# Performance work log

Hardware: AMD Instinct MI355X
Metric: run time of the kernel (lower is better)

The kernel has to match this reference:

```python
import jax, jax.numpy as jnp
import numpy as np

D_MODEL = 256
N_HEAD = 4
N_LAYERS = 2
D_FF = 4 * D_MODEL
VOCAB = 4096
DINO = 384
T_SEQ = 40
N_PATCH = 256
B = 32
LN_EPS = 1e-5


def setup_inputs() -> dict:
    key = jax.random.key(0)
    ks = jax.random.split(key, 24)
    f = jnp.float32
    d = {}
    d['patches'] = jax.random.normal(ks[0], (B, N_PATCH, DINO), dtype=f)
    d['tokens'] = jax.random.randint(ks[1], (B, T_SEQ), 0, VOCAB)
    s = 0.02
    d['embedding'] = jax.random.normal(ks[2], (VOCAB, D_MODEL), dtype=f) * s
    d['pos_emb'] = jax.random.normal(ks[3], (T_SEQ, D_MODEL), dtype=f) * s
    d['in_proj_w'] = jax.random.normal(ks[4], (N_LAYERS, 3 * D_MODEL, D_MODEL), dtype=f) * s
    d['in_proj_b'] = jnp.zeros((N_LAYERS, 3 * D_MODEL), dtype=f)
    d['out_proj_w'] = jax.random.normal(ks[5], (N_LAYERS, D_MODEL, D_MODEL), dtype=f) * s
    d['out_proj_b'] = jnp.zeros((N_LAYERS, D_MODEL), dtype=f)
    d['lin1_w'] = jax.random.normal(ks[6], (N_LAYERS, D_FF, D_MODEL), dtype=f) * s
    d['lin1_b'] = jnp.zeros((N_LAYERS, D_FF), dtype=f)
    d['lin2_w'] = jax.random.normal(ks[7], (N_LAYERS, D_MODEL, D_FF), dtype=f) * s
    d['lin2_b'] = jnp.zeros((N_LAYERS, D_MODEL), dtype=f)
    d['ln1_g'] = jnp.ones((N_LAYERS, D_MODEL), dtype=f)
    d['ln1_b'] = jnp.zeros((N_LAYERS, D_MODEL), dtype=f)
    d['ln2_g'] = jnp.ones((N_LAYERS, D_MODEL), dtype=f)
    d['ln2_b'] = jnp.zeros((N_LAYERS, D_MODEL), dtype=f)
    d['fus_w1'] = jax.random.normal(ks[8], (D_MODEL, DINO + D_MODEL), dtype=f) * s
    d['fus_b1'] = jnp.zeros((D_MODEL,), dtype=f)
    d['fus_w2'] = jax.random.normal(ks[9], (D_MODEL, D_MODEL), dtype=f) * s
    d['fus_b2'] = jnp.zeros((D_MODEL,), dtype=f)
    d['cls_w'] = jax.random.normal(ks[10], (VOCAB, D_MODEL), dtype=f) * s
    d['cls_b'] = jnp.zeros((VOCAB,), dtype=f)
    return d


def _layer_norm(x, g, b):
    m = jnp.mean(x, axis=-1, keepdims=True)
    v = jnp.mean((x - m) ** 2, axis=-1, keepdims=True)
    return (x - m) / jnp.sqrt(v + LN_EPS) * g + b


def _encode(x, mask, in_proj_w, in_proj_b, out_proj_w, out_proj_b,
            lin1_w, lin1_b, lin2_w, lin2_b, ln1_g, ln1_b, ln2_g, ln2_b):
    # x: [N, S, d], mask: [N, S] bool (True = valid key). Post-norm encoder, relu FFN.
    N, S, d = x.shape
    hd = d // N_HEAD
    for i in range(N_LAYERS):
        qkv = x @ in_proj_w[i].T + in_proj_b[i]
        q, k, v = jnp.split(qkv, 3, axis=-1)
        sh = lambda t: t.reshape(N, S, N_HEAD, hd).transpose(0, 2, 1, 3)
        q, k, v = sh(q), sh(k), sh(v)
        sc = jnp.einsum('nhqd,nhkd->nhqk', q, k) / np.sqrt(hd)
        sc = jnp.where(mask[:, None, None, :], sc, -1e9)
        a = jax.nn.softmax(sc, axis=-1)
        o = jnp.einsum('nhqk,nhkd->nhqd', a, v).transpose(0, 2, 1, 3).reshape(N, S, d)
        o = o @ out_proj_w[i].T + out_proj_b[i]
        x = _layer_norm(x + o, ln1_g[i], ln1_b[i])
        ff = jax.nn.relu(x @ lin1_w[i].T + lin1_b[i]) @ lin2_w[i].T + lin2_b[i]
        x = _layer_norm(x + ff, ln2_g[i], ln2_b[i])
    return x


def reference(patches, tokens, embedding, pos_emb, in_proj_w, in_proj_b,
              out_proj_w, out_proj_b, lin1_w, lin1_b, lin2_w, lin2_b,
              ln1_g, ln1_b, ln2_g, ln2_b, fus_w1, fus_b1, fus_w2, fus_b2,
              cls_w, cls_b):
    Bsz, T = tokens.shape
    d = embedding.shape[1]
    emb = embedding[tokens] + pos_emb[None, :T, :]      # [B, T, d]
    Tm1 = T - 1
    # All 39 prefix runs at once: prefix of length t+1 == full seq with keys > t masked.
    X = jnp.broadcast_to(emb[None], (Tm1, Bsz, T, d)).reshape(Tm1 * Bsz, T, d)
    valid = jnp.arange(T)[None, :] <= jnp.arange(Tm1)[:, None]  # [Tm1, T]
    mask = jnp.broadcast_to(valid[:, None, :], (Tm1, Bsz, T)).reshape(Tm1 * Bsz, T)
    enc = _encode(X, mask, in_proj_w, in_proj_b, out_proj_w, out_proj_b,
                  lin1_w, lin1_b, lin2_w, lin2_b, ln1_g, ln1_b, ln2_g, ln2_b)
    enc = enc.reshape(Tm1, Bsz, T, d)
    idx = jnp.arange(Tm1)
    ctx_rest = enc[idx, :, idx, :]                      # [Tm1, B, d] last valid position
    ctx = jnp.concatenate([jnp.zeros((1, Bsz, d), emb.dtype), ctx_rest], axis=0)  # [T, B, d]
    # Fusion MLP: split first linear into patch part (t-invariant) + context part.
    w1p, w1c = fus_w1[:, :DINO], fus_w1[:, DINO:]
    pp = jnp.einsum('bpd,kd->bpk', patches, w1p)        # [B, P, d]
    cp = jnp.einsum('tbd,kd->tbk', ctx, w1c) + fus_b1   # [T, B, d]
    h = jax.nn.gelu(pp[None] + cp[:, :, None, :], approximate=False)  # [T, B, P, d]
    feat = jnp.einsum('tbpk,mk->tbpm', h, fus_w2) + fus_b2            # [T, B, P, d]
    # Gather-only classification: prob of tokens[:, t] at step t.
    targets = tokens.T                                   # [T, B]
    cw = cls_w[targets]                                  # [T, B, d]
    cb = cls_b[targets]                                  # [T, B]
    logits = jnp.einsum('tbpm,tbm->tbp', feat, cw) + cb[:, :, None]
    probs = jax.nn.sigmoid(logits)                       # [T, B, P]
    return probs.transpose(1, 2, 0)                      # [B, P, T]
```

## Files before the change

kernel.cpp:

```cpp
#include <hip/hip_runtime.h>
#include <math.h>

#define DM    256
#define NH    4
#define HD    64
#define TS    40
#define TM1   39
#define BB    32
#define DFF   1024
#define DINO  384
#define NPATCH 256
#define VOCAB 4096

#define NTOK  24960
#define NQ2   1248

typedef _Float16 f16;
typedef __attribute__((ext_vector_type(8))) _Float16 half8;
typedef __attribute__((ext_vector_type(4))) _Float16 half4;
typedef __attribute__((ext_vector_type(4))) float f32x4;

#define OFF_EMBH   0u
#define OFF_EMB    163840u
#define OFF_QKVH   491520u
#define OFF_X1     983040u
#define OFF_X1H    7372800u
#define OFF_H1     10567680u
#define OFF_BIG    16957440u
#define   BT_AO1H  6389760u
#define   BT_X2    6553600u
#define   BT_X2H   6881280u
#define   BT_FF2H  7045120u
#define   BT_H1H   7700480u
#define OFF_CTX    29736960u
#define OFF_CPB    30064640u
#define OFF_U      30392320u
#define OFF_S      30720000u
#define OFF_WQKVH  30722048u
#define OFF_WQ1H   30820352u
#define OFF_KVWH   30853120u
#define OFF_WOH    30918656u
#define OFF_WOH1   30951424u
#define OFF_L1WH   30984192u
#define OFF_L1WH1  31115264u
#define OFF_L2WH   31246336u
#define OFF_L2WH1  31377408u
#define OFF_W1PH   31508480u
#define OFF_W1CH   31557632u
#define OFF_FW2TH  31590400u
#define OFF_CWGH   31623168u
#define OFF_MAP    31787008u
#define WS_FLOATS  31813216u

__global__ __launch_bounds__(256) void prep_kernel(
    const int* __restrict__ tokens, const float* __restrict__ etab,
    const float* __restrict__ pos,
    const float* __restrict__ ipw, const float* __restrict__ opw,
    const float* __restrict__ l1w, const float* __restrict__ l2w,
    const float* __restrict__ fw1, const float* __restrict__ fw2,
    const float* __restrict__ clsw, const float* __restrict__ clsb,
    const float* __restrict__ fb2,
    float* __restrict__ emb, f16* __restrict__ embh,
    f16* __restrict__ wqkvh, f16* __restrict__ wq1h, f16* __restrict__ kvwh,
    f16* __restrict__ woh, f16* __restrict__ woh1,
    f16* __restrict__ l1wh, f16* __restrict__ l1wh1,
    f16* __restrict__ l2wh, f16* __restrict__ l2wh1,
    f16* __restrict__ w1ph, f16* __restrict__ w1ch, f16* __restrict__ fw2th,
    f16* __restrict__ cwgh, float* __restrict__ sv, float* __restrict__ ctx,
    int* __restrict__ map1, int* __restrict__ map2)
{
    int i = blockIdx.x * 256 + threadIdx.x;
    if (i < 327680) {
        int r = i >> 8, j = i & 255;
        int p = r % TS;
        float v = etab[(size_t)tokens[r] * DM + j] + pos[p * DM + j];
        emb[i] = v; embh[i] = (f16)v;
        return;
    }
    i -= 327680;
    if (i < 196608) { wqkvh[i] = (f16)ipw[i]; return; }
    i -= 196608;
    if (i < 65536)  { wq1h[i] = (f16)ipw[196608 + i]; return; }
    i -= 65536;
    if (i < 131072) { kvwh[i] = (f16)ipw[262144 + i]; return; }
    i -= 131072;
    if (i < 65536)  { woh[i]  = (f16)opw[i]; return; }
    i -= 65536;
    if (i < 65536)  { woh1[i] = (f16)opw[65536 + i]; return; }
    i -= 65536;
    if (i < 262144) { l1wh[i]  = (f16)l1w[i]; return; }
    i -= 262144;
    if (i < 262144) { l1wh1[i] = (f16)l1w[262144 + i]; return; }
    i -= 262144;
    if (i < 262144) { l2wh[i]  = (f16)l2w[i]; return; }
    i -= 262144;
    if (i < 262144) { l2wh1[i] = (f16)l2w[262144 + i]; return; }
    i -= 262144;
    if (i < 98304) {
        int r = i / 384, c = i - r * 384;
        w1ph[i] = (f16)fw1[r * 640 + c];
        return;
    }
    i -= 98304;
    if (i < 65536) {
        int n = i >> 8, k = i & 255;
        w1ch[i] = (f16)fw1[n * 640 + 384 + k];
        return;
    }
    i -= 65536;
    if (i < 65536) {
        int j = i >> 8, k = i & 255;
        fw2th[i] = (f16)fw2[k * 256 + j];
        return;
    }
    i -= 65536;
    if (i < 327680) {
        int tb = i >> 8, j = i & 255;
        int t = tb >> 5, b = tb & 31;
        cwgh[i] = (f16)clsw[(size_t)tokens[b * TS + t] * DM + j];
        return;
    }
    i -= 327680;
    if (i < 81920) {
        int tb = i >> 6, l = i & 63;
        int t = tb >> 5, b = tb & 31;
        int tok = tokens[b * TS + t];
        float a = 0.f;
#pragma unroll
        for (int c = 0; c < 4; ++c)
            a += fb2[l + 64 * c] * clsw[(size_t)tok * DM + l + 64 * c];
#pragma unroll
        for (int o = 32; o; o >>= 1) a += __shfl_xor(a, o);
        if (l == 0) sv[tb] = a + clsb[tok];
        return;
    }
    i -= 81920;
    if (i < 8192) { ctx[i] = 0.f; return; }
    i -= 8192;
    if (i < NQ2) {
        int t = i >> 5, b = i & 31;
        map2[i] = ((t * (t + 1)) / 2 + t) * 32 + b;
    }
    if (i < NTOK) {
        int q = i >> 5, b = i & 31;
        int t = 0;
        while (((t + 1) * (t + 2)) / 2 <= q) ++t;
        int p = q - (t * (t + 1)) / 2;
        map1[i] = b * TS + p;
    }
}

__device__ __forceinline__ void stage16(const f16* g, f16* lbase_wave_uniform) {
    __builtin_amdgcn_global_load_lds(
        (const __attribute__((address_space(1))) void*)g,
        (__attribute__((address_space(3))) void*)lbase_wave_uniform, 16, 0, 0);
}

__device__ __forceinline__ half8 load_frag8(const float* p) {
    float4 a0 = *(const float4*)p;
    float4 a1 = *(const float4*)(p + 4);
    half8 h;
    h[0] = (f16)a0.x; h[1] = (f16)a0.y; h[2] = (f16)a0.z; h[3] = (f16)a0.w;
    h[4] = (f16)a1.x; h[5] = (f16)a1.y; h[6] = (f16)a1.z; h[7] = (f16)a1.w;
    return h;
}

template <int BM, typename TA, bool RELU, bool OUTF16>
__global__ __launch_bounds__(256) void gemm_x(
    const TA* __restrict__ A, int lda,
    const f16* __restrict__ B, int ldb,
    const float* __restrict__ bias,
    void* __restrict__ Cv, int ldc, int K)
{
    constexpr int AF  = BM / 8;
    constexpr int TF  = AF + 16;
    constexpr int MRE = BM / 32;
    constexpr int LPW = TF / 4;
    constexpr bool ASYNC = __is_same(TA, f16);
    constexpr int NBUF = ASYNC ? 2 : 1;
    __shared__ __align__(16) f16 lds[NBUF * TF * 512];
    int tid = threadIdx.x;
    int w = tid >> 6, l = tid & 63;
    int m0 = blockIdx.y * BM, n0 = blockIdx.x << 7;
    int lrow = l & 15;
    int lk8  = (l >> 4) << 3;
    int wm = w >> 1, wn = w & 1;

    f32x4 acc[MRE][4] = {};

    auto stage = [&](f16* dst, int k0) {
#pragma unroll
        for (int j = 0; j < TF / 4; ++j) {
            int f = (j << 2) | w;
            if (f < AF) {
                int mi = f >> 1, kc = f & 1;
                const TA* ga = A + (size_t)(m0 + (mi << 4) + lrow) * lda + k0 + (kc << 5) + lk8;
                if constexpr (ASYNC) {
                    stage16((const f16*)ga, dst + (f << 9));
                } else {
                    *(half8*)&dst[(f << 9) + (l << 3)] = load_frag8((const float*)ga);
                }
            } else {
                int fb = f - AF;
                int nj = fb >> 1, kc = fb & 1;
                const f16* gb = B + (size_t)(n0 + (nj << 4) + lrow) * ldb + k0 + (kc << 5) + lk8;
                stage16(gb, dst + (f << 9));
            }
        }
    };

    auto compute = [&](const f16* buf) {
#pragma unroll
        for (int kc = 0; kc < 2; ++kc) {
            half8 af[MRE], bfr[4];
#pragma unroll
            for (int i = 0; i < MRE; ++i)
                af[i] = *(const half8*)&buf[((((wm * MRE + i) << 1) | kc) << 9) + (l << 3)];
#pragma unroll
            for (int j2 = 0; j2 < 4; ++j2)
                bfr[j2] = *(const half8*)&buf[((AF + ((((wn << 2) | j2) << 1) | kc)) << 9) + (l << 3)];
#pragma unroll
            for (int i = 0; i < MRE; ++i)
#pragma unroll
                for (int j2 = 0; j2 < 4; ++j2)
                    acc[i][j2] = __builtin_amdgcn_mfma_f32_16x16x32_f16(
                        af[i], bfr[j2], acc[i][j2], 0, 0, 0);
        }
    };

    if constexpr (ASYNC) {
        int nk = K >> 6;
        stage(lds, 0);
        for (int t = 0; t < nk; ++t) {
            f16* cur = lds + (t & 1) * (TF * 512);
            if (t + 1 < nk) {
                stage(lds + ((t + 1) & 1) * (TF * 512), (t + 1) << 6);
                asm volatile("s_waitcnt vmcnt(%0)" :: "i"(LPW) : "memory");
            } else {
                asm volatile("s_waitcnt vmcnt(0)" ::: "memory");
            }
            __builtin_amdgcn_s_barrier();
            asm volatile("" ::: "memory");
            compute(cur);
            asm volatile("" ::: "memory");
            __builtin_amdgcn_s_barrier();
            asm volatile("" ::: "memory");
        }
    } else {
        for (int k0 = 0; k0 < K; k0 += 64) {
            stage(lds, k0);
            __syncthreads();
            compute(lds);
            __syncthreads();
        }
    }

    int colq = l & 15, rowq = (l >> 4) << 2;
#pragma unroll
    for (int i = 0; i < MRE; ++i) {
        int gmb = m0 + (wm * MRE + i) * 16 + rowq;
#pragma unroll
        for (int j2 = 0; j2 < 4; ++j2) {
            int gn = n0 + ((wn << 2) | j2) * 16 + colq;
            float bv = bias ? bias[gn] : 0.f;
#pragma unroll
            for (int r = 0; r < 4; ++r) {
                float v = acc[i][j2][r] + bv;
                if (RELU) v = fmaxf(v, 0.f);
                if (OUTF16)
                    ((f16*)Cv)[(size_t)(gmb + r) * ldc + gn] = (f16)v;
                else
                    ((float*)Cv)[(size_t)(gmb + r) * ldc + gn] = v;
            }
        }
    }
}

__global__ __launch_bounds__(256) void ln_kernel(
    float* __restrict__ X, const float* __restrict__ res,
    const int* __restrict__ map, const float* __restrict__ g,
    const float* __restrict__ beta, int nrows, f16* __restrict__ outh)
{
    int r = blockIdx.x * 4 + (threadIdx.x >> 6);
    if (r >= nrows) return;
    int l = threadIdx.x & 63;
    float* xp = X + (size_t)r * DM + l * 4;
    float4 v = *(float4*)xp;
    if (res) {
        int rr = map ? map[r] : r;
        float4 rv = *(const float4*)(res + (size_t)rr * DM + l * 4);
        v.x += rv.x; v.y += rv.y; v.z += rv.z; v.w += rv.w;
    }
    float s = v.x + v.y + v.z + v.w;
#pragma unroll
    for (int o = 32; o; o >>= 1) s += __shfl_xor(s, o);
    float mean = s * (1.f / 256.f);
    float dx = v.x - mean, dy = v.y - mean, dz = v.z - mean, dw = v.w - mean;
    float s2 = dx * dx + dy * dy + dz * dz + dw * dw;
#pragma unroll
    for (int o = 32; o; o >>= 1) s2 += __shfl_xor(s2, o);
    float rstd = 1.f / sqrtf(s2 * (1.f / 256.f) + 1e-5f);
    float4 gv = *(const float4*)(g + l * 4);
    float4 bv = *(const float4*)(beta + l * 4);
    float4 ov;
    ov.x = dx * rstd * gv.x + bv.x;
    ov.y = dy * rstd * gv.y + bv.y;
    ov.z = dz * rstd * gv.z + bv.z;
    ov.w = dw * rstd * gv.w + bv.w;
    *(float4*)xp = ov;
    if (outh) {
        half4 oh;
        oh[0] = (f16)ov.x; oh[1] = (f16)ov.y; oh[2] = (f16)ov.z; oh[3] = (f16)ov.w;
        *(half4*)(outh + (size_t)r * DM + l * 4) = oh;
    }
}

__global__ __launch_bounds__(256) void attn0_kernel(
    const f16* __restrict__ qkv, f16* __restrict__ ao)
{
    int bp = blockIdx.x;
    int b = bp / 39, p = bp % 39;
    int tid = threadIdx.x;
    int h = tid >> 6, l = tid & 63;

    float qv = (float)qkv[(size_t)(b * TS + p) * 768 + h * 64 + l];

    int krow = (l < 39) ? l : 38;
    const f16* Kr = qkv + (size_t)(b * TS + krow) * 768 + 256 + h * 64;
    float acc = 0.f;
#pragma unroll
    for (int c = 0; c < 8; ++c) {
        half8 k8 = *(const half8*)(Kr + c * 8);
#pragma unroll
        for (int j = 0; j < 8; ++j)
            acc += __shfl(qv, c * 8 + j) * (float)k8[j];
    }
    float s = acc * 0.125f;

    float m = -1e30f, lsum = 0.f, o = 0.f;
    for (int t = p; t < TM1; ++t) {
        float st = __shfl(s, t);
        float mnew = fmaxf(m, st);
        float c = __expf(m - mnew);
        float e = __expf(st - mnew);
        lsum = lsum * c + e;
        float vv = (float)qkv[(size_t)(b * TS + t) * 768 + 512 + h * 64 + l];
        o = o * c + e * vv;
        m = mnew;
        int row = ((t * (t + 1)) >> 1) + p;
        ao[((size_t)row * 32 + b) * DM + h * 64 + l] = (f16)(o / lsum);
    }
}

__global__ __launch_bounds__(256) void attn1_kernel(
    const float* __restrict__ h1, const f16* __restrict__ kv1,
    const f16* __restrict__ Wq, const float* __restrict__ bq,
    f16* __restrict__ ao1)
{
    int tb = blockIdx.x;
    int t = tb >> 5, b = tb & 31;
    int tid = threadIdx.x;
    int h = tid >> 6, l = tid & 63;
    int tri = (t * (t + 1)) >> 1;
    __shared__ float h1r[DM];
    h1r[tid] = h1[((size_t)(tri + t) * 32 + b) * DM + tid];
    __syncthreads();

    float q = bq[h * 64 + l];
    const half8* w8 = (const half8*)(Wq + (size_t)(h * 64 + l) * DM);
#pragma unroll 8
    for (int c = 0; c < 32; ++c) {
        half8 ww = w8[c];
#pragma unroll
        for (int j = 0; j < 8; ++j)
            q += (float)ww[j] * h1r[c * 8 + j];
    }

    int kr = (l <= t) ? l : t;
    const f16* Kp = kv1 + ((size_t)(tri + kr) * 32 + b) * 512 + h * 64;
    float sc = 0.f;
#pragma unroll
    for (int c = 0; c < 8; ++c) {
        half8 k8 = *(const half8*)(Kp + c * 8);
#pragma unroll
        for (int j = 0; j < 8; ++j)
            sc += __shfl(q, c * 8 + j) * (float)k8[j];
    }
    sc = (l <= t) ? sc * 0.125f : -1e30f;
    float m = sc;
#pragma unroll
    for (int o = 32; o; o >>= 1) m = fmaxf(m, __shfl_xor(m, o));
    float e = (l <= t) ? __expf(sc - m) : 0.f;
    float ss = e;
#pragma unroll
    for (int o = 32; o; o >>= 1) ss += __shfl_xor(ss, o);
    float a = e / ss;

    float o = 0.f;
    for (int k = 0; k <= t; ++k) {
        float ak = __shfl(a, k);
        o += ak * (float)kv1[((size_t)(tri + k) * 32 + b) * 512 + 256 + h * 64 + l];
    }
    ao1[(size_t)tb * DM + h * 64 + l] = (f16)o;
}

__device__ __forceinline__ float gelu_f(float x)
{
    float ax = fabsf(x);
    float z  = ax * 0.70710678118654752440f;
    float d  = 1.f + z * (0.278393f + z * (0.230389f + z * (0.000972f + z * 0.078108f)));
    float d2 = d * d;
    float E  = 1.f - __builtin_amdgcn_rcpf(d2 * d2);
    return 0.5f * x + 0.5f * ax * E;
}

__global__ __launch_bounds__(256) void final_out(
    const f16* __restrict__ pp, const float* __restrict__ cpb,
    const float* __restrict__ u, const float* __restrict__ sv,
    float* __restrict__ out)
{
    int bp = blockIdx.x;
    int b = bp >> 8;
    int tid = threadIdx.x;
    int w = tid >> 6, l = tid & 63;
    const f16* ppr = pp + (size_t)bp * DM + l * 4;
    float p0 = (float)ppr[0], p1 = (float)ppr[1];
    float p2 = (float)ppr[2], p3 = (float)ppr[3];
    for (int t = w; t < TS; t += 4) {
        int tb = t * 32 + b;
        float4 cp = *(const float4*)(cpb + (size_t)tb * DM + l * 4);
        float4 uu = *(const float4*)(u + (size_t)tb * DM + l * 4);
        float v = gelu_f(p0 + cp.x) * uu.x + gelu_f(p1 + cp.y) * uu.y +
                  gelu_f(p2 + cp.z) * uu.z + gelu_f(p3 + cp.w) * uu.w;
#pragma unroll
        for (int off = 32; off; off >>= 1) v += __shfl_xor(v, off);
        if (l == 0) out[(size_t)bp * TS + t] = 1.f / (1.f + __expf(-(v + sv[tb])));
    }
}

extern "C" void kernel_launch(void* const* d_in, const int* in_sizes, int n_in,
                              void* d_out, int out_size, void* d_ws, size_t ws_size,
                              hipStream_t stream)
{
    (void)in_sizes; (void)n_in; (void)out_size;
    const float* patches   = (const float*)d_in[0];
    const int*   tokens    = (const int*)  d_in[1];
    const float* embedding = (const float*)d_in[2];
    const float* pos_emb   = (const float*)d_in[3];
    const float* in_proj_w = (const float*)d_in[4];
    const float* in_proj_b = (const float*)d_in[5];
    const float* out_proj_w= (const float*)d_in[6];
    const float* out_proj_b= (const float*)d_in[7];
    const float* lin1_w    = (const float*)d_in[8];
    const float* lin1_b    = (const float*)d_in[9];
    const float* lin2_w    = (const float*)d_in[10];
    const float* lin2_b    = (const float*)d_in[11];
    const float* ln1_g     = (const float*)d_in[12];
    const float* ln1_b     = (const float*)d_in[13];
    const float* ln2_g     = (const float*)d_in[14];
    const float* ln2_b     = (const float*)d_in[15];
    const float* fus_w1    = (const float*)d_in[16];
    const float* fus_b1    = (const float*)d_in[17];
    const float* fus_w2    = (const float*)d_in[18];
    const float* fus_b2    = (const float*)d_in[19];
    const float* cls_w     = (const float*)d_in[20];
    const float* cls_b     = (const float*)d_in[21];

    if (ws_size < (size_t)WS_FLOATS * 4) return;

    float* ws   = (float*)d_ws;
    f16*   embh = (f16*)(ws + OFF_EMBH);
    float* emb  = ws + OFF_EMB;
    f16*   qkvh = (f16*)(ws + OFF_QKVH);
    float* x1   = ws + OFF_X1;
    f16*   x1h  = (f16*)(ws + OFF_X1H);
    f16*   pph  = (f16*)(ws + OFF_X1H);
    float* h1   = ws + OFF_H1;
    float* big  = ws + OFF_BIG;
    f16*   ao0h = (f16*)big;
    f16*   ff1h = (f16*)big;
    f16*   kv1h = (f16*)big;
    f16*   ao1h = (f16*)(big + BT_AO1H);
    float* x2   = big + BT_X2;
    f16*   x2h  = (f16*)(big + BT_X2H);
    f16*   ff2h = (f16*)(big + BT_FF2H);
    f16*   h1h  = (f16*)(big + BT_H1H);
    float* ctx  = ws + OFF_CTX;
    float* cpb  = ws + OFF_CPB;
    float* u    = ws + OFF_U;
    float* svec = ws + OFF_S;
    f16*   wqkvh= (f16*)(ws + OFF_WQKVH);
    f16*   wq1h = (f16*)(ws + OFF_WQ1H);
    f16*   kvwh = (f16*)(ws + OFF_KVWH);
    f16*   woh  = (f16*)(ws + OFF_WOH);
    f16*   woh1 = (f16*)(ws + OFF_WOH1);
    f16*   l1wh = (f16*)(ws + OFF_L1WH);
    f16*   l1wh1= (f16*)(ws + OFF_L1WH1);
    f16*   l2wh = (f16*)(ws + OFF_L2WH);
    f16*   l2wh1= (f16*)(ws + OFF_L2WH1);
    f16*   w1ph = (f16*)(ws + OFF_W1PH);
    f16*   w1ch = (f16*)(ws + OFF_W1CH);
    f16*   fw2th= (f16*)(ws + OFF_FW2TH);
    f16*   cwgh = (f16*)(ws + OFF_CWGH);
    int*   map1 = (int*)(ws + OFF_MAP);
    int*   map2 = map1 + NTOK;

    prep_kernel<<<10050, 256, 0, stream>>>(
        tokens, embedding, pos_emb, in_proj_w, out_proj_w, lin1_w, lin2_w,
        fus_w1, fus_w2, cls_w, cls_b, fus_b2,
        emb, embh, wqkvh, wq1h, kvwh, woh, woh1, l1wh, l1wh1, l2wh, l2wh1,
        w1ph, w1ch, fw2th, cwgh, svec, ctx, map1, map2);

    gemm_x<64, f16, false, false><<<dim3(2, 20), 256, 0, stream>>>(
        cwgh, DM, fw2th, DM, nullptr, u, DM, DM);

    gemm_x<64, f16, false, true><<<dim3(6, 20), 256, 0, stream>>>(
        embh, DM, wqkvh, DM, in_proj_b, qkvh, 768, DM);
    attn0_kernel<<<NQ2, 256, 0, stream>>>(qkvh, ao0h);
    gemm_x<64, f16, false, false><<<dim3(2, 390), 256, 0, stream>>>(
        ao0h, DM, woh, DM, out_proj_b, x1, DM, DM);
    ln_kernel<<<6240, 256, 0, stream>>>(x1, emb, map1, ln1_g, ln1_b, NTOK, x1h);
    gemm_x<128, f16, true, true><<<dim3(8, 195), 256, 0, stream>>>(
        x1h, DM, l1wh, DM, lin1_b, ff1h, DFF, DM);
    gemm_x<64, f16, false, false><<<dim3(2, 390), 256, 0, stream>>>(
        ff1h, DFF, l2wh, DFF, lin2_b, h1, DM, DFF);
    ln_kernel<<<6240, 256, 0, stream>>>(h1, x1, nullptr, ln2_g, ln2_b, NTOK, h1h);

    gemm_x<64, float, false, true><<<dim3(2, 128), 256, 0, stream>>>(
        patches, DINO, w1ph, DINO, nullptr, pph, DM, DINO);

    gemm_x<128, f16, false, true><<<dim3(4, 195), 256, 0, stream>>>(
        h1h, DM, kvwh, DM, in_proj_b + 768 + 256, kv1h, 512, DM);
    attn1_kernel<<<NQ2, 256, 0, stream>>>(
        h1, kv1h, wq1h, in_proj_b + 768, ao1h);
    gemm_x<64, f16, false, false><<<dim3(2, 20), 256, 0, stream>>>(
        ao1h, DM, woh1, DM, out_proj_b + DM, x2, DM, DM);
    ln_kernel<<<312, 256, 0, stream>>>(x2, h1, map2, ln1_g + DM, ln1_b + DM, NQ2, x2h);
    gemm_x<64, f16, true, true><<<dim3(8, 20), 256, 0, stream>>>(
        x2h, DM, l1wh1, DM, lin1_b + DFF, ff2h, DFF, DM);
    gemm_x<64, f16, false, false><<<dim3(2, 20), 256, 0, stream>>>(
        ff2h, DFF, l2wh1, DFF, lin2_b + DM, ctx + BB * DM, DM, DFF);
    ln_kernel<<<312, 256, 0, stream>>>(ctx + BB * DM, x2, nullptr, ln2_g + DM, ln2_b + DM, NQ2, nullptr);

    gemm_x<64, float, false, false><<<dim3(2, 20), 256, 0, stream>>>(
        ctx, DM, w1ch, DM, fus_b1, cpb, DM, DM);

    final_out<<<BB * NPATCH, 256, 0, stream>>>(pph, cpb, u, svec, (float*)d_out);
}
```

Baseline: 447.1 us.

## Restructure final GELU-dot kernel to tile patches per lane with LDS transpose

The final output kernel now assigns one patch per lane, 64 patches per block and 8 timesteps per block, instead of one block per (b,patch) doing a wave-wide reduction per timestep. Patch features are transposed into LDS so each lane reads its own row, while the context and u vectors are read at wave-uniform addresses that broadcast across lanes. This removes the per-timestep shuffle reductions and the repeated global loads of cp/u per patch. In exchange it launches far fewer blocks (640) and does long serial per-lane loops, which may lower occupancy and latency hiding.

```diff
diff --git a/kernel.cpp b/kernel.cpp
--- a/kernel.cpp
+++ b/kernel.cpp
@@ -419,23 +419,57 @@
     const float* __restrict__ u, const float* __restrict__ sv,
     float* __restrict__ out)
 {
-    int bp = blockIdx.x;
-    int b = bp >> 8;
+    int blk = blockIdx.x;
+    int b  = blk / 20;
+    int rr = blk - b * 20;
+    int pg = rr / 5;
+    int tg = rr - pg * 5;
     int tid = threadIdx.x;
     int w = tid >> 6, l = tid & 63;
-    const f16* ppr = pp + (size_t)bp * DM + l * 4;
-    float p0 = (float)ppr[0], p1 = (float)ppr[1];
-    float p2 = (float)ppr[2], p3 = (float)ppr[3];
-    for (int t = w; t < TS; t += 4) {
-        int tb = t * 32 + b;
-        float4 cp = *(const float4*)(cpb + (size_t)tb * DM + l * 4);
-        float4 uu = *(const float4*)(u + (size_t)tb * DM + l * 4);
-        float v = gelu_f(p0 + cp.x) * uu.x + gelu_f(p1 + cp.y) * uu.y +
-                  gelu_f(p2 + cp.z) * uu.z + gelu_f(p3 + cp.w) * uu.w;
-#pragma unroll
-        for (int off = 32; off; off >>= 1) v += __shfl_xor(v, off);
-        if (l == 0) out[(size_t)bp * TS + t] = 1.f / (1.f + __expf(-(v + sv[tb])));
-    }
+
+    __shared__ unsigned ldsT[128 * 64];
+
+    {
+        const f16* rowp = pp + (size_t)((b << 8) + (pg << 6) + l) * DM + (w << 6);
+#pragma unroll
+        for (int j = 0; j < 8; ++j) {
+            half8 h8 = *(const half8*)(rowp + j * 8);
+#pragma unroll
+            for (int j2 = 0; j2 < 4; ++j2) {
+                union { f16 h[2]; unsigned v; } cv;
+                cv.h[0] = h8[j2 * 2]; cv.h[1] = h8[j2 * 2 + 1];
+                int k2 = (w << 5) + (j << 2) + j2;
+                ldsT[(k2 << 6) + l] = cv.v;
+            }
+        }
+    }
+    __syncthreads();
+
+    int t0  = tg * 8 + w * 2;
+    int tb0 = __builtin_amdgcn_readfirstlane(t0 * 32 + b);
+    int tb1 = tb0 + 32;
+    const float* cpa = cpb + (size_t)tb0 * DM;
+    const float* cpc = cpb + (size_t)tb1 * DM;
+    const float* ua  = u + (size_t)tb0 * DM;
+    const float* uc  = u + (size_t)tb1 * DM;
+
+    float acc0 = 0.f, acc1 = 0.f;
+#pragma unroll 4
+    for (int k2 = 0; k2 < 128; ++k2) {
+        union { unsigned v; f16 h[2]; } pr;
+        pr.v = ldsT[(k2 << 6) + l];
+        float a0 = (float)pr.h[0], a1 = (float)pr.h[1];
+        float2 c0 = *(const float2*)(cpa + (k2 << 1));
+        float2 c1 = *(const float2*)(cpc + (k2 << 1));
+        float2 u0 = *(const float2*)(ua + (k2 << 1));
+        float2 u1 = *(const float2*)(uc + (k2 << 1));
+        acc0 += gelu_f(a0 + c0.x) * u0.x + gelu_f(a1 + c0.y) * u0.y;
+        acc1 += gelu_f(a0 + c1.x) * u1.x + gelu_f(a1 + c1.y) * u1.y;
+    }
+    float s0 = sv[tb0], s1 = sv[tb1];
+    int op = ((b << 8) + (pg << 6) + l) * TS;
+    out[op + t0]     = 1.f / (1.f + __expf(-(acc0 + s0)));
+    out[op + t0 + 1] = 1.f / (1.f + __expf(-(acc1 + s1)));
 }
 
 extern "C" void kernel_launch(void* const* d_in, const int* in_sizes, int n_in,
@@ -545,5 +579,5 @@
     gemm_x<64, float, false, false><<<dim3(2, 20), 256, 0, stream>>>(
         ctx, DM, w1ch, DM, fus_b1, cpb, DM, DM);
 
-    final_out<<<BB * NPATCH, 256, 0, stream>>>(pph, cpb, u, svec, (float*)d_out);
-}
+    final_out<<<640, 256, 0, stream>>>(pph, cpb, u, svec, (float*)d_out);
+}
```

Result: no change. 444.8 us (-0.5%).
